# Kernel optimization log

Hardware: AMD Instinct MI355X
Metric: run time of the kernel (lower is better)

## Reference

```python
import jax, jax.numpy as jnp
import numpy as np

# dims (match init_kwargs config)
B, IMG, P, G = 8, 224, 16, 14
N = G * G          # 196 patches
PD = P * P         # 256 patch dim
D, DFF, L, C = 128, 256, 2, 1000
SCALE = 0.05


def trop_mm(x, W):
    # y[..., i] = max_j (x[..., j] + W[i, j])  (tropical mat-vec)
    return jnp.max(x[..., None, :] + W, axis=-1)


def pnorm(x):
    # projective normalize; max constant is detached in the original
    return x - jax.lax.stop_gradient(jnp.max(x, axis=-1, keepdims=True))


def attention(x, qW, kW, vW):
    q = trop_mm(x, qW)
    k = trop_mm(x, kW)
    v = trop_mm(x, vW)
    # score_ij = max_d (q_id + k_jd)  -> (B, N, N)
    scores = jnp.max(q[:, :, None, :] + k[:, None, :, :], axis=-1)
    scores = scores - jnp.max(scores, axis=-1, keepdims=True)
    # out_id = max_j (score_ij + v_jd)
    return jnp.max(scores[..., None] + v[:, None, :, :], axis=2)


def block(x, qW, kW, vW, f1W, f2W, tau):
    xn = pnorm(x)
    a = pnorm(attention(xn, qW, kW, vW))
    x = jnp.maximum(x, a)                 # tropical residual
    xn = pnorm(x)
    h = trop_mm(xn, f1W)
    h = jnp.maximum(h, tau)               # tropical ReLU, tau shape (1,)
    ff = pnorm(trop_mm(h, f2W))
    return jnp.maximum(x, ff)


def setup_inputs() -> dict:
    key = jax.random.key(0)
    ks = jax.random.split(key, 32)
    d = {"x": jax.random.normal(ks[0], (B, IMG, IMG), jnp.float32)}
    d["embed_W"] = jax.random.normal(ks[1], (D, PD), jnp.float32) * SCALE
    d["pos"] = jax.random.normal(ks[2], (N, D), jnp.float32) * SCALE
    i = 3
    for l in range(L):
        for nm, shp in (("q_W", (D, D)), ("k_W", (D, D)), ("v_W", (D, D)), ("ff1_W", (DFF, D)), ("ff2_W", (D, DFF))):
            d[f"{nm}{l}"] = jax.random.normal(ks[i], shp, jnp.float32) * SCALE
            i += 1
        d[f"tau{l}"] = jnp.array([-2.0], jnp.float32)
    d["head_W"] = jax.random.normal(ks[i], (C, D), jnp.float32) * SCALE
    d["logit_scale"] = jnp.array(10.0, jnp.float32)
    return d


def reference(x, embed_W, pos, q_W0, k_W0, v_W0, ff1_W0, ff2_W0, tau0,
              q_W1, k_W1, v_W1, ff1_W1, ff2_W1, tau1, head_W, logit_scale):
    # patchify: (B, 224, 224) -> (B, 196, 256)
    patches = x.reshape(B, G, P, G, P).transpose(0, 1, 3, 2, 4).reshape(B, N, PD)
    h = trop_mm(patches, embed_W) + pos[None]
    layers = ((q_W0, k_W0, v_W0, ff1_W0, ff2_W0, tau0),
              (q_W1, k_W1, v_W1, ff1_W1, ff2_W1, tau1))
    for qW, kW, vW, f1, f2, tau in layers:
        h = block(h, qW, kW, vW, f1, f2, tau)
    pooled = jnp.max(h, axis=1)          # tropical global pool over patches
    return trop_mm(pooled, head_W) * logit_scale   # (B, C)
```

## Files before the change

### kernel.cpp

```cpp
#include <hip/hip_runtime.h>
#include <math.h>

#define BDIM 8
#define IMG 224
#define PP 16
#define GG 14
#define NN 196
#define PD 256
#define DD 128
#define DFFV 256
#define CC 1000

#define NEGINF (-INFINITY)

#define WT4_EW    0
#define WT4_QKV0  8192
#define WT4_QKV1  20480
#define WT4_F1_0  32768
#define WT4_F1_1  40960
#define WT4_F2_0  49152
#define WT4_F2_1  57344
#define WT4_HW    65536
#define WT4_TOTAL 97536
#define WT_FLOATS (WT4_TOTAL * 4)

__device__ __forceinline__ unsigned keyenc(float f) {
  unsigned u = __float_as_uint(f);
  return (u & 0x80000000u) ? ~u : (u | 0x80000000u);
}
__device__ __forceinline__ float keydec(unsigned k) {
  unsigned u = (k & 0x80000000u) ? (k & 0x7fffffffu) : ~k;
  return __uint_as_float(u);
}

__global__ __launch_bounds__(256) void transpose_weights_kernel(
    const float* __restrict__ eW, const float* __restrict__ qW0,
    const float* __restrict__ kW0, const float* __restrict__ vW0,
    const float* __restrict__ qW1, const float* __restrict__ kW1,
    const float* __restrict__ vW1, const float* __restrict__ f1W0,
    const float* __restrict__ f1W1, const float* __restrict__ f2W0,
    const float* __restrict__ f2W1, const float* __restrict__ hW,
    float* __restrict__ wt) {
  int idx = blockIdx.x * 256 + threadIdx.x;
  float4* wt4 = reinterpret_cast<float4*>(wt);
  const float* src;
  float4* dst;
  int local, OUT, J;
  if (idx < 8192) {
    src = eW; dst = wt4 + WT4_EW; local = idx; OUT = 128; J = 256;
  } else if (idx < 32768) {
    int s = (idx - 8192) >> 12; local = (idx - 8192) & 4095;
    src = (s == 0) ? qW0 : (s == 1) ? kW0 : (s == 2) ? vW0
        : (s == 3) ? qW1 : (s == 4) ? kW1 : vW1;
    dst = wt4 + WT4_QKV0 + s * 4096; OUT = 128; J = 128;
  } else if (idx < 49152) {
    int s = (idx - 32768) >> 13; local = (idx - 32768) & 8191;
    src = s ? f1W1 : f1W0; dst = wt4 + WT4_F1_0 + s * 8192; OUT = 256; J = 128;
  } else if (idx < 65536) {
    int s = (idx - 49152) >> 13; local = (idx - 49152) & 8191;
    src = s ? f2W1 : f2W0; dst = wt4 + WT4_F2_0 + s * 8192; OUT = 128; J = 256;
  } else if (idx < WT4_TOTAL) {
    src = hW; dst = wt4 + WT4_HW; local = idx - 65536; OUT = 1000; J = 128;
  } else {
    return;
  }
  int o, j4;
  if (OUT == 128) { o = local & 127; j4 = local >> 7; }
  else if (OUT == 256) { o = local & 255; j4 = local >> 8; }
  else { o = local % 1000; j4 = local / 1000; }
  dst[local] = *reinterpret_cast<const float4*>(src + (size_t)o * J + j4 * 4);
}

__global__ __launch_bounds__(384) void embed_qkv_kernel(
    const float* __restrict__ x, const float* __restrict__ wt,
    const float* __restrict__ pos, float* __restrict__ h,
    float* __restrict__ qg, float* __restrict__ KT, float* __restrict__ vg,
    unsigned* __restrict__ poolkey) {
  int nt = blockIdx.x, b = blockIdx.y, n0 = nt * 4;
  __shared__ float patch[4][PD];
  __shared__ float hrow[4][DD];
  __shared__ float mxs[4];
  int t = threadIdx.x;
  const float4* wt4 = reinterpret_cast<const float4*>(wt);
  if (nt == 0 && t < DD) poolkey[b * DD + t] = 0u;
  if (t < 256) {
    int p = t >> 6, r = t & 63, pi = r >> 2, pj4 = r & 3;
    int n = n0 + p, gi = n / GG, gj = n % GG;
    float4 val = *reinterpret_cast<const float4*>(
        x + (size_t)(b * IMG + gi * PP + pi) * IMG + gj * PP + pj4 * 4);
    *reinterpret_cast<float4*>(&patch[p][pi * PP + pj4 * 4]) = val;
  }
  __syncthreads();
  if (t < 256) {
    int half = t >> 7, d = t & 127;
    int p0 = half * 2, p1 = p0 + 1;
    float a0 = NEGINF, a1 = NEGINF;
    const float4* W4 = wt4 + WT4_EW;
#pragma unroll 4
    for (int j4 = 0; j4 < PD / 4; j4++) {
      float4 w = W4[j4 * DD + d];
      a0 = fmaxf(a0, patch[p0][j4 * 4 + 0] + w.x); a0 = fmaxf(a0, patch[p0][j4 * 4 + 1] + w.y);
      a0 = fmaxf(a0, patch[p0][j4 * 4 + 2] + w.z); a0 = fmaxf(a0, patch[p0][j4 * 4 + 3] + w.w);
      a1 = fmaxf(a1, patch[p1][j4 * 4 + 0] + w.x); a1 = fmaxf(a1, patch[p1][j4 * 4 + 1] + w.y);
      a1 = fmaxf(a1, patch[p1][j4 * 4 + 2] + w.z); a1 = fmaxf(a1, patch[p1][j4 * 4 + 3] + w.w);
    }
    float h0 = a0 + pos[(size_t)(n0 + p0) * DD + d];
    float h1v = a1 + pos[(size_t)(n0 + p1) * DD + d];
    hrow[p0][d] = h0; hrow[p1][d] = h1v;
    h[(size_t)(b * NN + n0 + p0) * DD + d] = h0;
    h[(size_t)(b * NN + n0 + p1) * DD + d] = h1v;
  }
  __syncthreads();
  if (t < 128) {
    int r = t >> 5, l = t & 31;
    float m = fmaxf(fmaxf(hrow[r][l], hrow[r][l + 32]), fmaxf(hrow[r][l + 64], hrow[r][l + 96]));
#pragma unroll
    for (int mask = 16; mask >= 1; mask >>= 1) m = fmaxf(m, __shfl_xor(m, mask));
    if (l == 0) mxs[r] = m;
  }
  __syncthreads();
  {
    int m = t >> 7, i = t & 127;
    const float4* W4 = wt4 + WT4_QKV0 + m * 4096;
    float acc[4];
#pragma unroll
    for (int r = 0; r < 4; r++) acc[r] = NEGINF;
#pragma unroll 4
    for (int j4 = 0; j4 < DD / 4; j4++) {
      float4 w = W4[j4 * DD + i];
#pragma unroll
      for (int r = 0; r < 4; r++) {
        acc[r] = fmaxf(acc[r], hrow[r][j4 * 4 + 0] + w.x);
        acc[r] = fmaxf(acc[r], hrow[r][j4 * 4 + 1] + w.y);
        acc[r] = fmaxf(acc[r], hrow[r][j4 * 4 + 2] + w.z);
        acc[r] = fmaxf(acc[r], hrow[r][j4 * 4 + 3] + w.w);
      }
    }
    if (m == 0) {
#pragma unroll
      for (int r = 0; r < 4; r++)
        qg[(size_t)(b * NN + n0 + r) * DD + i] = acc[r] - mxs[r];
    } else if (m == 1) {
#pragma unroll
      for (int r = 0; r < 4; r++)
        KT[(((size_t)b * 32 + (i >> 2)) * NN + (n0 + r)) * 4 + (i & 3)] =
            acc[r] - mxs[r];
    } else {
#pragma unroll
      for (int r = 0; r < 4; r++)
        vg[(size_t)(b * NN + n0 + r) * DD + i] = acc[r] - mxs[r];
    }
  }
}

__global__ __launch_bounds__(384) void layer_kernel(
    const float* __restrict__ qg, const float* __restrict__ KTin,
    const float* __restrict__ vg, float* __restrict__ h,
    const float* __restrict__ wt, int f1off, int f2off,
    const float* __restrict__ tau, int qkvoff_next, float* __restrict__ qo,
    float* __restrict__ KTo, float* __restrict__ vo,
    unsigned* __restrict__ poolkey) {
  int nt = blockIdx.x, b = blockIdx.y, i0 = nt * 4;
  __shared__ float qs[4][DD];
  __shared__ float hrow[4][DD];
  __shared__ float sc[4][NN];
  __shared__ float h1s[4][DFFV];
  __shared__ float scratch[12 * 4 * DD];
  __shared__ float red[2][4];
  __shared__ float mxs[4];
  int t = threadIdx.x;
  const float4* wt4 = reinterpret_cast<const float4*>(wt);
  if (t < 128) {
    float4 val = reinterpret_cast<const float4*>(qg + (size_t)(b * NN + i0) * DD)[t];
    *reinterpret_cast<float4*>(&qs[0][0] + t * 4) = val;
  } else if (t < 256) {
    int tt = t - 128;
    float4 val = reinterpret_cast<const float4*>(h + (size_t)(b * NN + i0) * DD)[tt];
    *reinterpret_cast<float4*>(&hrow[0][0] + tt * 4) = val;
  }
  __syncthreads();
  if (t < NN) {
    const float4* KT4 = reinterpret_cast<const float4*>(KTin);
    float s0 = NEGINF, s1 = NEGINF, s2 = NEGINF, s3 = NEGINF;
#pragma unroll 4
    for (int d4 = 0; d4 < DD / 4; d4++) {
      float4 kv = KT4[((size_t)b * 32 + d4) * NN + t];
      s0 = fmaxf(s0, qs[0][d4 * 4 + 0] + kv.x); s0 = fmaxf(s0, qs[0][d4 * 4 + 1] + kv.y);
      s0 = fmaxf(s0, qs[0][d4 * 4 + 2] + kv.z); s0 = fmaxf(s0, qs[0][d4 * 4 + 3] + kv.w);
      s1 = fmaxf(s1, qs[1][d4 * 4 + 0] + kv.x); s1 = fmaxf(s1, qs[1][d4 * 4 + 1] + kv.y);
      s1 = fmaxf(s1, qs[1][d4 * 4 + 2] + kv.z); s1 = fmaxf(s1, qs[1][d4 * 4 + 3] + kv.w);
      s2 = fmaxf(s2, qs[2][d4 * 4 + 0] + kv.x); s2 = fmaxf(s2, qs[2][d4 * 4 + 1] + kv.y);
      s2 = fmaxf(s2, qs[2][d4 * 4 + 2] + kv.z); s2 = fmaxf(s2, qs[2][d4 * 4 + 3] + kv.w);
      s3 = fmaxf(s3, qs[3][d4 * 4 + 0] + kv.x); s3 = fmaxf(s3, qs[3][d4 * 4 + 1] + kv.y);
      s3 = fmaxf(s3, qs[3][d4 * 4 + 2] + kv.z); s3 = fmaxf(s3, qs[3][d4 * 4 + 3] + kv.w);
    }
    sc[0][t] = s0; sc[1][t] = s1; sc[2][t] = s2; sc[3][t] = s3;
  }
  __syncthreads();
  {
    int d4 = t & 31, jg = t >> 5;
    float4 o0 = {NEGINF, NEGINF, NEGINF, NEGINF};
    float4 o1 = o0, o2 = o0, o3 = o0;
#pragma unroll 4
    for (int j = jg; j < NN; j += 12) {
      float4 vv = *reinterpret_cast<const float4*>(vg + (size_t)(b * NN + j) * DD + d4 * 4);
      float c0 = sc[0][j], c1 = sc[1][j], c2 = sc[2][j], c3 = sc[3][j];
      o0.x = fmaxf(o0.x, c0 + vv.x); o0.y = fmaxf(o0.y, c0 + vv.y);
      o0.z = fmaxf(o0.z, c0 + vv.z); o0.w = fmaxf(o0.w, c0 + vv.w);
      o1.x = fmaxf(o1.x, c1 + vv.x); o1.y = fmaxf(o1.y, c1 + vv.y);
      o1.z = fmaxf(o1.z, c1 + vv.z); o1.w = fmaxf(o1.w, c1 + vv.w);
      o2.x = fmaxf(o2.x, c2 + vv.x); o2.y = fmaxf(o2.y, c2 + vv.y);
      o2.z = fmaxf(o2.z, c2 + vv.z); o2.w = fmaxf(o2.w, c2 + vv.w);
      o3.x = fmaxf(o3.x, c3 + vv.x); o3.y = fmaxf(o3.y, c3 + vv.y);
      o3.z = fmaxf(o3.z, c3 + vv.z); o3.w = fmaxf(o3.w, c3 + vv.w);
    }
    *reinterpret_cast<float4*>(&scratch[((jg * 4 + 0) << 7) + d4 * 4]) = o0;
    *reinterpret_cast<float4*>(&scratch[((jg * 4 + 1) << 7) + d4 * 4]) = o1;
    *reinterpret_cast<float4*>(&scratch[((jg * 4 + 2) << 7) + d4 * 4]) = o2;
    *reinterpret_cast<float4*>(&scratch[((jg * 4 + 3) << 7) + d4 * 4]) = o3;
  }
  __syncthreads();
  float oacc[4];
  if (t < 128) {
    int lane = t & 63, wv = t >> 6;
#pragma unroll
    for (int r = 0; r < 4; r++) {
      float m = scratch[(r << 7) + t];
#pragma unroll
      for (int g = 1; g < 12; g++) m = fmaxf(m, scratch[((g * 4 + r) << 7) + t]);
      oacc[r] = m;
      float mv = m;
#pragma unroll
      for (int mask = 32; mask >= 1; mask >>= 1) mv = fmaxf(mv, __shfl_xor(mv, mask));
      if (lane == 0) red[wv][r] = mv;
    }
  }
  __syncthreads();
  if (t < 128) {
#pragma unroll
    for (int r = 0; r < 4; r++) {
      float omax = fmaxf(red[0][r], red[1][r]);
      hrow[r][t] = fmaxf(hrow[r][t], oacc[r] - omax);
    }
  }
  __syncthreads();
  if (t < 128) {
    int r = t >> 5, l = t & 31;
    float m = fmaxf(fmaxf(hrow[r][l], hrow[r][l + 32]), fmaxf(hrow[r][l + 64], hrow[r][l + 96]));
#pragma unroll
    for (int mask = 16; mask >= 1; mask >>= 1) m = fmaxf(m, __shfl_xor(m, mask));
    if (l == 0) mxs[r] = m;
  }
  __syncthreads();
  if (t < DFFV) {
    float tv = tau[0];
    const float4* W4 = wt4 + f1off;
    float acc[4];
#pragma unroll
    for (int r = 0; r < 4; r++) acc[r] = NEGINF;
#pragma unroll 4
    for (int j4 = 0; j4 < DD / 4; j4++) {
      float4 w = W4[j4 * DFFV + t];
#pragma unroll
      for (int r = 0; r < 4; r++) {
        acc[r] = fmaxf(acc[r], hrow[r][j4 * 4 + 0] + w.x);
        acc[r] = fmaxf(acc[r], hrow[r][j4 * 4 + 1] + w.y);
        acc[r] = fmaxf(acc[r], hrow[r][j4 * 4 + 2] + w.z);
        acc[r] = fmaxf(acc[r], hrow[r][j4 * 4 + 3] + w.w);
      }
    }
#pragma unroll
    for (int r = 0; r < 4; r++) h1s[r][t] = fmaxf(acc[r] - mxs[r], tv);
  }
  __syncthreads();
  if (t < DFFV) {
    int i = t & 127, jh = t >> 7;
    const float4* W4 = wt4 + f2off;
    float acc[4];
#pragma unroll
    for (int r = 0; r < 4; r++) acc[r] = NEGINF;
#pragma unroll 4
    for (int j4 = 0; j4 < 32; j4++) {
      float4 w = W4[(jh * 32 + j4) * DD + i];
      int jb = jh * 128 + j4 * 4;
#pragma unroll
      for (int r = 0; r < 4; r++) {
        acc[r] = fmaxf(acc[r], h1s[r][jb + 0] + w.x);
        acc[r] = fmaxf(acc[r], h1s[r][jb + 1] + w.y);
        acc[r] = fmaxf(acc[r], h1s[r][jb + 2] + w.z);
        acc[r] = fmaxf(acc[r], h1s[r][jb + 3] + w.w);
      }
    }
#pragma unroll
    for (int r = 0; r < 4; r++) scratch[((jh * 4 + r) << 7) + i] = acc[r];
  }
  __syncthreads();
  float fm[4];
  if (t < 128) {
    int lane = t & 63, wv = t >> 6;
#pragma unroll
    for (int r = 0; r < 4; r++) {
      fm[r] = fmaxf(scratch[(r << 7) + t], scratch[((4 + r) << 7) + t]);
      float mv = fm[r];
#pragma unroll
      for (int mask = 32; mask >= 1; mask >>= 1) mv = fmaxf(mv, __shfl_xor(mv, mask));
      if (lane == 0) red[wv][r] = mv;
    }
  }
  __syncthreads();
  if (qkvoff_next < 0) {
    if (t < 128) {
      float pool = NEGINF;
#pragma unroll
      for (int r = 0; r < 4; r++) {
        float omax = fmaxf(red[0][r], red[1][r]);
        pool = fmaxf(pool, fmaxf(hrow[r][t], fm[r] - omax));
      }
      atomicMax(&poolkey[b * DD + t], keyenc(pool));
    }
    return;
  }
  if (t < 128) {
    int lane = t & 63, wv = t >> 6;
#pragma unroll
    for (int r = 0; r < 4; r++) {
      float omax = fmaxf(red[0][r], red[1][r]);
      float nh = fmaxf(hrow[r][t], fm[r] - omax);
      hrow[r][t] = nh;
      h[(size_t)(b * NN + i0 + r) * DD + t] = nh;
      float mv = nh;
#pragma unroll
      for (int mask = 32; mask >= 1; mask >>= 1) mv = fmaxf(mv, __shfl_xor(mv, mask));
      if (lane == 0) red[wv][r] = mv;
    }
  }
  __syncthreads();
  {
    int m = t >> 7, i = t & 127;
    const float4* W4 = wt4 + qkvoff_next + m * 4096;
    float acc[4], mx[4];
#pragma unroll
    for (int r = 0; r < 4; r++) {
      acc[r] = NEGINF;
      mx[r] = fmaxf(red[0][r], red[1][r]);
    }
#pragma unroll 4
    for (int j4 = 0; j4 < DD / 4; j4++) {
      float4 w = W4[j4 * DD + i];
#pragma unroll
      for (int r = 0; r < 4; r++) {
        acc[r] = fmaxf(acc[r], hrow[r][j4 * 4 + 0] + w.x);
        acc[r] = fmaxf(acc[r], hrow[r][j4 * 4 + 1] + w.y);
        acc[r] = fmaxf(acc[r], hrow[r][j4 * 4 + 2] + w.z);
        acc[r] = fmaxf(acc[r], hrow[r][j4 * 4 + 3] + w.w);
      }
    }
    if (m == 0) {
#pragma unroll
      for (int r = 0; r < 4; r++)
        qo[(size_t)(b * NN + i0 + r) * DD + i] = acc[r] - mx[r];
    } else if (m == 1) {
#pragma unroll
      for (int r = 0; r < 4; r++)
        KTo[(((size_t)b * 32 + (i >> 2)) * NN + (i0 + r)) * 4 + (i & 3)] =
            acc[r] - mx[r];
    } else {
#pragma unroll
      for (int r = 0; r < 4; r++)
        vo[(size_t)(b * NN + i0 + r) * DD + i] = acc[r] - mx[r];
    }
  }
}

__global__ __launch_bounds__(128) void head_kernel(
    const unsigned* __restrict__ poolkey, const float* __restrict__ wt,
    const float* __restrict__ lscale, float* __restrict__ out) {
  int cb = blockIdx.x, b = blockIdx.y;
  __shared__ float pooled[DD];
  int t = threadIdx.x;
  const float4* W4 = reinterpret_cast<const float4*>(wt) + WT4_HW;
  pooled[t] = keydec(poolkey[b * DD + t]);
  __syncthreads();
  if (t < 125) {
    int c = cb * 125 + t;
    float acc = NEGINF;
#pragma unroll 4
    for (int k4 = 0; k4 < DD / 4; k4++) {
      float4 w = W4[k4 * CC + c];
      acc = fmaxf(acc, pooled[k4 * 4 + 0] + w.x);
      acc = fmaxf(acc, pooled[k4 * 4 + 1] + w.y);
      acc = fmaxf(acc, pooled[k4 * 4 + 2] + w.z);
      acc = fmaxf(acc, pooled[k4 * 4 + 3] + w.w);
    }
    out[(size_t)b * CC + c] = acc * lscale[0];
  }
}

extern "C" void kernel_launch(void* const* d_in, const int* in_sizes, int n_in,
                              void* d_out, int out_size, void* d_ws, size_t ws_size,
                              hipStream_t stream) {
  const float* x = (const float*)d_in[0];
  const float* embed_W = (const float*)d_in[1];
  const float* pos = (const float*)d_in[2];
  const float* qW0 = (const float*)d_in[3];
  const float* kW0 = (const float*)d_in[4];
  const float* vW0 = (const float*)d_in[5];
  const float* f1W0 = (const float*)d_in[6];
  const float* f2W0 = (const float*)d_in[7];
  const float* tau0 = (const float*)d_in[8];
  const float* qW1 = (const float*)d_in[9];
  const float* kW1 = (const float*)d_in[10];
  const float* vW1 = (const float*)d_in[11];
  const float* f1W1 = (const float*)d_in[12];
  const float* f2W1 = (const float*)d_in[13];
  const float* tau1 = (const float*)d_in[14];
  const float* headW = (const float*)d_in[15];
  const float* lscale = (const float*)d_in[16];
  float* out = (float*)d_out;

  float* ws = (float*)d_ws;
  size_t o = 0;
  float* h = ws + o; o += (size_t)BDIM * NN * DD;
  float* qb = ws + o; o += (size_t)BDIM * NN * DD;
  float* KT1 = ws + o; o += (size_t)BDIM * NN * DD;
  float* vb = ws + o; o += (size_t)BDIM * NN * DD;
  float* KT2 = ws + o; o += (size_t)BDIM * NN * DD;
  float* v2 = ws + o; o += (size_t)BDIM * NN * DD;
  unsigned* poolkey = (unsigned*)(ws + o); o += (size_t)BDIM * DD;
  float* wt = ws + o; o += (size_t)WT_FLOATS;

  transpose_weights_kernel<<<dim3(WT4_TOTAL / 256 + 1), 256, 0, stream>>>(
      embed_W, qW0, kW0, vW0, qW1, kW1, vW1, f1W0, f1W1, f2W0, f2W1, headW, wt);
  embed_qkv_kernel<<<dim3(49, BDIM), 384, 0, stream>>>(
      x, wt, pos, h, qb, KT1, vb, poolkey);
  layer_kernel<<<dim3(49, BDIM), 384, 0, stream>>>(
      qb, KT1, vb, h, wt, WT4_F1_0, WT4_F2_0, tau0, WT4_QKV1, qb, KT2, v2,
      poolkey);
  layer_kernel<<<dim3(49, BDIM), 384, 0, stream>>>(
      qb, KT2, v2, h, wt, WT4_F1_1, WT4_F2_1, tau1, -1, nullptr, nullptr,
      nullptr, poolkey);
  head_kernel<<<dim3(8, BDIM), 128, 0, stream>>>(poolkey, wt, lscale, out);
}
```

Measured before the change: 154.9 us.

## Fuse classification head into last layer kernel via last-block counter

Removes the separate head kernel launch by having the last block per batch item (detected through an atomic done counter) compute the tropical head projection inside the final layer kernel. Pool-key and counter initialisation moves into the weight-transpose kernel. This saves a launch and inter-kernel gap but serialises the head work for each batch onto a single block at the tail and adds fences and atomics.

```diff
diff --git a/kernel.cpp b/kernel.cpp
--- a/kernel.cpp
+++ b/kernel.cpp
@@ -40,8 +40,13 @@
     const float* __restrict__ vW1, const float* __restrict__ f1W0,
     const float* __restrict__ f1W1, const float* __restrict__ f2W0,
     const float* __restrict__ f2W1, const float* __restrict__ hW,
-    float* __restrict__ wt) {
+    float* __restrict__ wt, unsigned* __restrict__ poolkey,
+    unsigned* __restrict__ done) {
   int idx = blockIdx.x * 256 + threadIdx.x;
+  if (blockIdx.x == 0 && threadIdx.x < BDIM) done[threadIdx.x] = 0u;
+  if (blockIdx.x == 1) {
+    for (int i = threadIdx.x; i < BDIM * DD; i += 256) poolkey[i] = 0u;
+  }
   float4* wt4 = reinterpret_cast<float4*>(wt);
   const float* src;
   float4* dst;
@@ -74,15 +79,13 @@
 __global__ __launch_bounds__(384) void embed_qkv_kernel(
     const float* __restrict__ x, const float* __restrict__ wt,
     const float* __restrict__ pos, float* __restrict__ h,
-    float* __restrict__ qg, float* __restrict__ KT, float* __restrict__ vg,
-    unsigned* __restrict__ poolkey) {
+    float* __restrict__ qg, float* __restrict__ KT, float* __restrict__ vg) {
   int nt = blockIdx.x, b = blockIdx.y, n0 = nt * 4;
   __shared__ float patch[4][PD];
   __shared__ float hrow[4][DD];
   __shared__ float mxs[4];
   int t = threadIdx.x;
   const float4* wt4 = reinterpret_cast<const float4*>(wt);
-  if (nt == 0 && t < DD) poolkey[b * DD + t] = 0u;
   if (t < 256) {
     int p = t >> 6, r = t & 63, pi = r >> 2, pj4 = r & 3;
     int n = n0 + p, gi = n / GG, gj = n % GG;
@@ -159,7 +162,8 @@
     const float* __restrict__ wt, int f1off, int f2off,
     const float* __restrict__ tau, int qkvoff_next, float* __restrict__ qo,
     float* __restrict__ KTo, float* __restrict__ vo,
-    unsigned* __restrict__ poolkey) {
+    unsigned* __restrict__ poolkey, unsigned* __restrict__ done,
+    const float* __restrict__ lscale, float* __restrict__ out) {
   int nt = blockIdx.x, b = blockIdx.y, i0 = nt * 4;
   __shared__ float qs[4][DD];
   __shared__ float hrow[4][DD];
@@ -168,6 +172,8 @@
   __shared__ float scratch[12 * 4 * DD];
   __shared__ float red[2][4];
   __shared__ float mxs[4];
+  __shared__ float pooled[DD];
+  __shared__ unsigned lastflag;
   int t = threadIdx.x;
   const float4* wt4 = reinterpret_cast<const float4*>(wt);
   if (t < 128) {
@@ -318,6 +324,31 @@
       }
       atomicMax(&poolkey[b * DD + t], keyenc(pool));
     }
+    __syncthreads();
+    if (t == 0) {
+      __threadfence();
+      lastflag = atomicAdd(&done[b], 1u);
+    }
+    __syncthreads();
+    if (lastflag == 48u) {
+      __threadfence();
+      if (t < DD) pooled[t] = keydec(atomicOr(&poolkey[b * DD + t], 0u));
+      __syncthreads();
+      float ls = lscale[0];
+      const float4* W4 = wt4 + WT4_HW;
+      for (int c = t; c < CC; c += 384) {
+        float acc = NEGINF;
+#pragma unroll 4
+        for (int k4 = 0; k4 < DD / 4; k4++) {
+          float4 w = W4[k4 * CC + c];
+          acc = fmaxf(acc, pooled[k4 * 4 + 0] + w.x);
+          acc = fmaxf(acc, pooled[k4 * 4 + 1] + w.y);
+          acc = fmaxf(acc, pooled[k4 * 4 + 2] + w.z);
+          acc = fmaxf(acc, pooled[k4 * 4 + 3] + w.w);
+        }
+        out[(size_t)b * CC + c] = acc * ls;
+      }
+    }
     return;
   }
   if (t < 128) {
@@ -369,30 +400,6 @@
       for (int r = 0; r < 4; r++)
         vo[(size_t)(b * NN + i0 + r) * DD + i] = acc[r] - mx[r];
     }
-  }
-}
-
-__global__ __launch_bounds__(128) void head_kernel(
-    const unsigned* __restrict__ poolkey, const float* __restrict__ wt,
-    const float* __restrict__ lscale, float* __restrict__ out) {
-  int cb = blockIdx.x, b = blockIdx.y;
-  __shared__ float pooled[DD];
-  int t = threadIdx.x;
-  const float4* W4 = reinterpret_cast<const float4*>(wt) + WT4_HW;
-  pooled[t] = keydec(poolkey[b * DD + t]);
-  __syncthreads();
-  if (t < 125) {
-    int c = cb * 125 + t;
-    float acc = NEGINF;
-#pragma unroll 4
-    for (int k4 = 0; k4 < DD / 4; k4++) {
-      float4 w = W4[k4 * CC + c];
-      acc = fmaxf(acc, pooled[k4 * 4 + 0] + w.x);
-      acc = fmaxf(acc, pooled[k4 * 4 + 1] + w.y);
-      acc = fmaxf(acc, pooled[k4 * 4 + 2] + w.z);
-      acc = fmaxf(acc, pooled[k4 * 4 + 3] + w.w);
-    }
-    out[(size_t)b * CC + c] = acc * lscale[0];
   }
 }
 
@@ -427,17 +434,18 @@
   float* KT2 = ws + o; o += (size_t)BDIM * NN * DD;
   float* v2 = ws + o; o += (size_t)BDIM * NN * DD;
   unsigned* poolkey = (unsigned*)(ws + o); o += (size_t)BDIM * DD;
+  unsigned* done = (unsigned*)(ws + o); o += 8;
   float* wt = ws + o; o += (size_t)WT_FLOATS;
 
   transpose_weights_kernel<<<dim3(WT4_TOTAL / 256 + 1), 256, 0, stream>>>(
-      embed_W, qW0, kW0, vW0, qW1, kW1, vW1, f1W0, f1W1, f2W0, f2W1, headW, wt);
+      embed_W, qW0, kW0, vW0, qW1, kW1, vW1, f1W0, f1W1, f2W0, f2W1, headW,
+      wt, poolkey, done);
   embed_qkv_kernel<<<dim3(49, BDIM), 384, 0, stream>>>(
-      x, wt, pos, h, qb, KT1, vb, poolkey);
+      x, wt, pos, h, qb, KT1, vb);
   layer_kernel<<<dim3(49, BDIM), 384, 0, stream>>>(
       qb, KT1, vb, h, wt, WT4_F1_0, WT4_F2_0, tau0, WT4_QKV1, qb, KT2, v2,
-      poolkey);
+      poolkey, done, lscale, out);
   layer_kernel<<<dim3(49, BDIM), 384, 0, stream>>>(
       qb, KT2, v2, h, wt, WT4_F1_1, WT4_F2_1, tau1, -1, nullptr, nullptr,
-      nullptr, poolkey);
-  head_kernel<<<dim3(8, BDIM), 128, 0, stream>>>(poolkey, wt, lscale, out);
-}
+      nullptr, poolkey, done, lscale, out);
+}
```

Result: slower. 168.2 us (+8.6%).
